# Optimization experiments

Measured on AMD Instinct MI355X. Metric: run time of the kernel, lower is better.

The kernel has to match this reference:

```python
import jax, jax.numpy as jnp
import numpy as np

N, E, IN_F, H, F = 4096, 131072, 512, 8, 32  # n_nodes, n_edges, in_features, n_heads, n_hidden
SLOPE = 0.2


def setup_inputs() -> dict:
    key = jax.random.key(0)
    k1, k2, k3, k4 = jax.random.split(key, 4)
    h = jax.random.normal(k1, (N, IN_F), dtype=jnp.float32)
    edge_index = jax.random.randint(k2, (2, E), 0, N)
    train_mask = jnp.ones((E + N,), dtype=jnp.float32)  # mask values written into adj (incl. self-loops appended in forward)
    W_fc = jax.random.normal(k3, (IN_F, H * F), dtype=jnp.float32) * (1.0 / np.sqrt(IN_F))
    W_attn = jax.random.normal(k4, (2 * F,), dtype=jnp.float32) * (1.0 / np.sqrt(2 * F))
    return {"h": h, "edge_index": edge_index, "train_mask": train_mask, "W_fc": W_fc, "W_attn": W_attn}


def reference(h, edge_index, train_mask, W_fc, W_attn):
    n = h.shape[0]
    g = (h @ W_fc).reshape(n, H, F)  # [n, H, F]
    # attn_fc(concat(g_i, g_j)) == g_i @ W_attn[:F] + g_j @ W_attn[F:]  (same math, no NxNx2F tensor)
    el = g @ W_attn[:F]  # [n, H], contribution of source row i
    er = g @ W_attn[F:]  # [n, H], contribution of column j
    e = jax.nn.leaky_relu(el[:, None, :] + er[None, :, :], SLOPE)  # [n, n, H]
    # adjacency: edges (+ self-loops appended in forward) get train_mask values, then diagonal forced to 1
    src = jnp.concatenate([edge_index[0], jnp.arange(n)])
    dst = jnp.concatenate([edge_index[1], jnp.arange(n)])
    adj = jnp.zeros((n, n), dtype=h.dtype).at[src, dst].set(train_mask)
    diag = jnp.arange(n)
    adj = adj.at[diag, diag].set(1.0)
    e = jnp.where(adj[:, :, None] == 0, -jnp.inf, e)
    a = jax.nn.softmax(e, axis=1)  # softmax over neighbors j (dropout p=0 -> identity)
    attn_res = jnp.einsum('ijh,jhf->ihf', a, g)  # [n, H, F]
    return attn_res.reshape(n, H * F)  # is_concat=True
```

## Files before the change

kernel.cpp:

```cpp
#include <hip/hip_runtime.h>
#include <stdint.h>

#define NN   4096
#define NE   131072
#define KIN  512
#define NH   8
#define HF   256
#define SLOPE 0.2f

typedef __attribute__((ext_vector_type(8))) short bf16x8;
typedef __attribute__((ext_vector_type(4))) float f32x4;


__device__ __forceinline__ unsigned short f2bf(float x) {
  unsigned u = __builtin_bit_cast(unsigned, x);
  u += 0x7FFFu + ((u >> 16) & 1u);
  return (unsigned short)(u >> 16);
}
__device__ __forceinline__ float bf2f(unsigned short x) {
  unsigned u = ((unsigned)x) << 16;
  return __builtin_bit_cast(float, u);
}

__global__ __launch_bounds__(256) void prep_k(const float* __restrict__ A,
                                              const float* __restrict__ B,
                                              unsigned* __restrict__ bitmap,
                                              unsigned short* __restrict__ Abf,
                                              unsigned short* __restrict__ Btbf) {
  __shared__ float tile[32][33];
  const int b = blockIdx.x, t = threadIdx.x;
  if (b < 512) {
    ((float4*)bitmap)[b * 256 + t] = make_float4(0.f, 0.f, 0.f, 0.f);
  } else if (b < 2560) {
    size_t idx = ((size_t)(b - 512) * 256 + t) * 4;
    float4 v = *(const float4*)&A[idx];
    ushort4 o;
    o.x = f2bf(v.x); o.y = f2bf(v.y); o.z = f2bf(v.z); o.w = f2bf(v.w);
    *(ushort4*)&Abf[idx] = o;
  } else {
    int bb = b - 2560;
    int k0 = (bb >> 3) * 32, n0 = (bb & 7) * 32;
    int lr = t >> 3, lc = (t & 7) * 4;
    float4 v = *(const float4*)&B[(size_t)(k0 + lr) * HF + n0 + lc];
    tile[lr][lc] = v.x; tile[lr][lc + 1] = v.y; tile[lr][lc + 2] = v.z; tile[lr][lc + 3] = v.w;
    __syncthreads();
    ushort4 o;
    o.x = f2bf(tile[lc + 0][lr]); o.y = f2bf(tile[lc + 1][lr]);
    o.z = f2bf(tile[lc + 2][lr]); o.w = f2bf(tile[lc + 3][lr]);
    *(ushort4*)&Btbf[(size_t)(n0 + lr) * KIN + k0 + lc] = o;
  }
}

__global__ __launch_bounds__(256) void gemm_adj_k(const unsigned short* __restrict__ A,
                                                  const unsigned short* __restrict__ Bt,
                                                  const float* __restrict__ Wa,
                                                  unsigned short* __restrict__ gbf,
                                                  float* __restrict__ el,
                                                  float* __restrict__ er,
                                                  const int* __restrict__ ei,
                                                  const float* __restrict__ mask,
                                                  unsigned* __restrict__ bitmap) {
  __shared__ unsigned short smem[2][4096];
  const int bx = blockIdx.x, t = threadIdx.x;
  if (bx >= 1024) {
    int k = (bx - 1024) * 256 + t;
    int s, d; float m;
    if (k < NE) { s = ei[k]; d = ei[NE + k]; m = mask[k]; }
    else        { s = k - NE; d = s; m = 1.0f; }
    if (m != 0.0f) atomicOr(&bitmap[s * 128 + (d >> 5)], 1u << (d & 31));
    return;
  }
  const int gx = bx & 127, gy = bx >> 7;
  const int row0 = gx * 32, col0 = gy * 32;
  const int w = t >> 6, l = t & 63;
  const int wr = w >> 1, wc = w & 1;

  const int srow = (w << 3) + (l >> 3);
  const int sch  = (l & 7) ^ (srow & 7);
  const unsigned short* gA = &A[(size_t)(row0 + srow) * KIN + sch * 8];
  const unsigned short* gB = &Bt[(size_t)(col0 + srow) * KIN + sch * 8];

#define STAGE(bf, ks)                                                                             \
  do {                                                                                            \
    __builtin_amdgcn_global_load_lds(                                                             \
        (const __attribute__((address_space(1))) unsigned int*)(gA + (size_t)(ks) * 64),          \
        (__attribute__((address_space(3))) unsigned int*)(&smem[bf][w * 512]), 16, 0, 0);         \
    __builtin_amdgcn_global_load_lds(                                                             \
        (const __attribute__((address_space(1))) unsigned int*)(gB + (size_t)(ks) * 64),          \
        (__attribute__((address_space(3))) unsigned int*)(&smem[bf][2048 + w * 512]), 16, 0, 0);  \
  } while (0)

  f32x4 acc = {};
  STAGE(0, 0);
  __syncthreads();
  const int lrow = l & 15, kg = l >> 4;
  const int ar = wr * 16 + lrow, br = wc * 16 + lrow;
  for (int ks = 0; ks < 8; ++ks) {
    const int bf = ks & 1;
    if (ks < 7) STAGE(bf ^ 1, ks + 1);
    bf16x8 a0 = *(const bf16x8*)&smem[bf][ar * 64 + ((kg ^ (ar & 7)) << 3)];
    bf16x8 a1 = *(const bf16x8*)&smem[bf][ar * 64 + (((4 + kg) ^ (ar & 7)) << 3)];
    bf16x8 b0 = *(const bf16x8*)&smem[bf][2048 + br * 64 + ((kg ^ (br & 7)) << 3)];
    bf16x8 b1 = *(const bf16x8*)&smem[bf][2048 + br * 64 + (((4 + kg) ^ (br & 7)) << 3)];
    acc = __builtin_amdgcn_mfma_f32_16x16x32_bf16(a0, b0, acc, 0, 0, 0);
    acc = __builtin_amdgcn_mfma_f32_16x16x32_bf16(a1, b1, acc, 0, 0, 0);
    __syncthreads();
  }
#undef STAGE

  const int crow = (l >> 4) * 4, ccol = l & 15;
  const int gr0 = row0 + wr * 16 + crow, gc = col0 + wc * 16 + ccol;
#pragma unroll
  for (int q = 0; q < 4; ++q) gbf[(size_t)(gr0 + q) * HF + gc] = f2bf(acc[q]);

  float* red = (float*)smem;
  const int f = wc * 16 + ccol;
  const float wal = Wa[f], war = Wa[32 + f];
#pragma unroll
  for (int q = 0; q < 4; ++q) {
    float pel = acc[q] * wal, per = acc[q] * war;
#pragma unroll
    for (int m = 8; m >= 1; m >>= 1) { pel += __shfl_xor(pel, m); per += __shfl_xor(per, m); }
    if (ccol == 0) {
      int rl = wr * 16 + crow + q;
      red[wc * 32 + rl] = pel;
      red[64 + wc * 32 + rl] = per;
    }
  }
  __syncthreads();
  if (t < 32) {
    el[(row0 + t) * NH + gy] = red[t] + red[32 + t];
    er[(row0 + t) * NH + gy] = red[64 + t] + red[96 + t];
  }
}

__global__ __launch_bounds__(256) void attn_k(const unsigned* __restrict__ bitmap,
                                              const unsigned short* __restrict__ gbf,
                                              const float* __restrict__ el_,
                                              const float* __restrict__ er_,
                                              float* __restrict__ out) {
  __shared__ unsigned short jl[NN];
  __shared__ float wlds[256 * NH];
  __shared__ int wtot[4];
  __shared__ int totalS;

  const int i = blockIdx.x;
  const int t = threadIdx.x;
  const int lane = t & 63;

  unsigned wbits = 0; int cnt = 0;
  if (t < 128) { wbits = bitmap[i * 128 + t]; cnt = __popc(wbits); }
  int incl = cnt;
#pragma unroll
  for (int d = 1; d < 64; d <<= 1) {
    int u = __shfl_up(incl, d);
    if (lane >= d) incl += u;
  }
  if (lane == 63) wtot[t >> 6] = incl;
  __syncthreads();
  int base = (t >= 64 && t < 128) ? wtot[0] : 0;
  if (t == 127) totalS = base + incl;
  if (t < 128) {
    int off = base + incl - cnt;
    unsigned ww = wbits;
    while (ww) {
      int b = __ffs(ww) - 1;
      jl[off++] = (unsigned short)(t * 32 + b);
      ww &= ww - 1;
    }
  }
  __syncthreads();
  const int total = totalS;

  const int hh = t >> 5;
  float acc = 0.f, den = 0.f;
  for (int c0 = 0; c0 < total; c0 += 256) {
    const int CL = min(256, total - c0);
    for (int p = t; p < CL * NH; p += 256) {
      int k = p >> 3, h2 = p & 7;
      int j = jl[c0 + k];
      float e  = el_[i * NH + h2] + er_[(size_t)j * NH + h2];
      float lr = e > 0.f ? e : SLOPE * e;
      wlds[p] = __expf(lr);
    }
    __syncthreads();
    int k = 0;
    for (; k + 4 <= CL; k += 4) {
      int j0 = jl[c0 + k], j1 = jl[c0 + k + 1], j2 = jl[c0 + k + 2], j3 = jl[c0 + k + 3];
      float g0 = bf2f(gbf[(size_t)j0 * HF + t]);
      float g1 = bf2f(gbf[(size_t)j1 * HF + t]);
      float g2 = bf2f(gbf[(size_t)j2 * HF + t]);
      float g3 = bf2f(gbf[(size_t)j3 * HF + t]);
      float w0 = wlds[(k + 0) * NH + hh], w1 = wlds[(k + 1) * NH + hh];
      float w2 = wlds[(k + 2) * NH + hh], w3 = wlds[(k + 3) * NH + hh];
      den += (w0 + w1) + (w2 + w3);
      acc += w0 * g0; acc += w1 * g1; acc += w2 * g2; acc += w3 * g3;
    }
    for (; k < CL; ++k) {
      int j0 = jl[c0 + k];
      float w0 = wlds[k * NH + hh];
      den += w0;
      acc += w0 * bf2f(gbf[(size_t)j0 * HF + t]);
    }
    __syncthreads();
  }
  out[(size_t)i * HF + t] = acc / den;
}

extern "C" void kernel_launch(void* const* d_in, const int* in_sizes, int n_in,
                              void* d_out, int out_size, void* d_ws, size_t ws_size,
                              hipStream_t stream) {
  const float* h      = (const float*)d_in[0];
  const int*   ei     = (const int*)d_in[1];
  const float* mask   = (const float*)d_in[2];
  const float* W_fc   = (const float*)d_in[3];
  const float* W_attn = (const float*)d_in[4];
  float* out = (float*)d_out;

  char* ws = (char*)d_ws;
  unsigned* bitmap      = (unsigned*)ws;
  unsigned short* gbf   = (unsigned short*)(ws + (size_t)2 * 1024 * 1024);
  float* el             = (float*)(ws + (size_t)4 * 1024 * 1024);
  float* er             = (float*)(ws + (size_t)4 * 1024 * 1024 + 128 * 1024);
  unsigned short* Abf   = (unsigned short*)(ws + (size_t)4 * 1024 * 1024 + 256 * 1024);
  unsigned short* Btbf  = (unsigned short*)(ws + (size_t)8 * 1024 * 1024 + 256 * 1024);

  prep_k<<<2688, 256, 0, stream>>>(h, W_fc, bitmap, Abf, Btbf);
  gemm_adj_k<<<1024 + 528, 256, 0, stream>>>(Abf, Btbf, W_attn, gbf, el, er, ei, mask, bitmap);
  attn_k<<<NN, 256, 0, stream>>>(bitmap, gbf, el, er, out);
}
```

Baseline: 37.03 us.

## Fuse fp32-to-bf16 conversion of h into GEMM and use one wave per node in attention

The GEMM now loads h as fp32 directly, converts it to bf16 in registers and writes it to LDS. This removes the separate prep pass over A, along with its 4 MB of writes and reads. The attention kernel now assigns one wavefront per node, with each lane covering 4 features. It computes the softmax weight inline per neighbour and drops the block-level LDS weight staging and its barriers. The trade-off is that every lane recomputes exp for its head, and the A loads move into the register-staged GEMM loop.

```diff
diff --git a/kernel.cpp b/kernel.cpp
--- a/kernel.cpp
+++ b/kernel.cpp
@@ -21,24 +21,19 @@
   unsigned u = ((unsigned)x) << 16;
   return __builtin_bit_cast(float, u);
 }
-
-__global__ __launch_bounds__(256) void prep_k(const float* __restrict__ A,
-                                              const float* __restrict__ B,
+__device__ __forceinline__ unsigned pack2(float lo, float hi) {
+  return (unsigned)f2bf(lo) | ((unsigned)f2bf(hi) << 16);
+}
+
+__global__ __launch_bounds__(256) void prep_k(const float* __restrict__ B,
                                               unsigned* __restrict__ bitmap,
-                                              unsigned short* __restrict__ Abf,
                                               unsigned short* __restrict__ Btbf) {
   __shared__ float tile[32][33];
   const int b = blockIdx.x, t = threadIdx.x;
   if (b < 512) {
     ((float4*)bitmap)[b * 256 + t] = make_float4(0.f, 0.f, 0.f, 0.f);
-  } else if (b < 2560) {
-    size_t idx = ((size_t)(b - 512) * 256 + t) * 4;
-    float4 v = *(const float4*)&A[idx];
-    ushort4 o;
-    o.x = f2bf(v.x); o.y = f2bf(v.y); o.z = f2bf(v.z); o.w = f2bf(v.w);
-    *(ushort4*)&Abf[idx] = o;
   } else {
-    int bb = b - 2560;
+    int bb = b - 512;
     int k0 = (bb >> 3) * 32, n0 = (bb & 7) * 32;
     int lr = t >> 3, lc = (t & 7) * 4;
     float4 v = *(const float4*)&B[(size_t)(k0 + lr) * HF + n0 + lc];
@@ -51,7 +46,7 @@
   }
 }
 
-__global__ __launch_bounds__(256) void gemm_adj_k(const unsigned short* __restrict__ A,
+__global__ __launch_bounds__(256) void gemm_adj_k(const float* __restrict__ h,
                                                   const unsigned short* __restrict__ Bt,
                                                   const float* __restrict__ Wa,
                                                   unsigned short* __restrict__ gbf,
@@ -76,37 +71,52 @@
   const int wr = w >> 1, wc = w & 1;
 
   const int srow = (w << 3) + (l >> 3);
-  const int sch  = (l & 7) ^ (srow & 7);
-  const unsigned short* gA = &A[(size_t)(row0 + srow) * KIN + sch * 8];
-  const unsigned short* gB = &Bt[(size_t)(col0 + srow) * KIN + sch * 8];
-
-#define STAGE(bf, ks)                                                                             \
-  do {                                                                                            \
-    __builtin_amdgcn_global_load_lds(                                                             \
-        (const __attribute__((address_space(1))) unsigned int*)(gA + (size_t)(ks) * 64),          \
-        (__attribute__((address_space(3))) unsigned int*)(&smem[bf][w * 512]), 16, 0, 0);         \
-    __builtin_amdgcn_global_load_lds(                                                             \
-        (const __attribute__((address_space(1))) unsigned int*)(gB + (size_t)(ks) * 64),          \
-        (__attribute__((address_space(3))) unsigned int*)(&smem[bf][2048 + w * 512]), 16, 0, 0);  \
-  } while (0)
+  const int sc   = l & 7;
+  const int aoff = srow * 64 + ((sc ^ (srow & 7)) << 3);
+  const float* gA = &h[(size_t)(row0 + srow) * KIN + sc * 8];
+  const int schB = sc ^ (srow & 7);
+  const unsigned short* gB = &Bt[(size_t)(col0 + srow) * KIN + schB * 8];
+
+#define BSTAGE(bf, ks)                                                                            \
+  __builtin_amdgcn_global_load_lds(                                                               \
+      (const __attribute__((address_space(1))) unsigned int*)(gB + (size_t)(ks) * 64),            \
+      (__attribute__((address_space(3))) unsigned int*)(&smem[bf][2048 + w * 512]), 16, 0, 0)
 
   f32x4 acc = {};
-  STAGE(0, 0);
+  {
+    float4 va0 = *(const float4*)(gA);
+    float4 va1 = *(const float4*)(gA + 4);
+    BSTAGE(0, 0);
+    uint4 w4 = {pack2(va0.x, va0.y), pack2(va0.z, va0.w),
+                pack2(va1.x, va1.y), pack2(va1.z, va1.w)};
+    *(uint4*)&smem[0][aoff] = w4;
+  }
   __syncthreads();
+
   const int lrow = l & 15, kg = l >> 4;
   const int ar = wr * 16 + lrow, br = wc * 16 + lrow;
   for (int ks = 0; ks < 8; ++ks) {
     const int bf = ks & 1;
-    if (ks < 7) STAGE(bf ^ 1, ks + 1);
+    float4 na0, na1;
+    if (ks < 7) {
+      na0 = *(const float4*)(gA + (ks + 1) * 64);
+      na1 = *(const float4*)(gA + (ks + 1) * 64 + 4);
+      BSTAGE(bf ^ 1, ks + 1);
+    }
     bf16x8 a0 = *(const bf16x8*)&smem[bf][ar * 64 + ((kg ^ (ar & 7)) << 3)];
     bf16x8 a1 = *(const bf16x8*)&smem[bf][ar * 64 + (((4 + kg) ^ (ar & 7)) << 3)];
     bf16x8 b0 = *(const bf16x8*)&smem[bf][2048 + br * 64 + ((kg ^ (br & 7)) << 3)];
     bf16x8 b1 = *(const bf16x8*)&smem[bf][2048 + br * 64 + (((4 + kg) ^ (br & 7)) << 3)];
     acc = __builtin_amdgcn_mfma_f32_16x16x32_bf16(a0, b0, acc, 0, 0, 0);
     acc = __builtin_amdgcn_mfma_f32_16x16x32_bf16(a1, b1, acc, 0, 0, 0);
+    if (ks < 7) {
+      uint4 w4 = {pack2(na0.x, na0.y), pack2(na0.z, na0.w),
+                  pack2(na1.x, na1.y), pack2(na1.z, na1.w)};
+      *(uint4*)&smem[bf ^ 1][aoff] = w4;
+    }
     __syncthreads();
   }
-#undef STAGE
+#undef BSTAGE
 
   const int crow = (l >> 4) * 4, ccol = l & 15;
   const int gr0 = row0 + wr * 16 + crow, gc = col0 + wc * 16 + ccol;
@@ -139,72 +149,47 @@
                                               const float* __restrict__ el_,
                                               const float* __restrict__ er_,
                                               float* __restrict__ out) {
-  __shared__ unsigned short jl[NN];
-  __shared__ float wlds[256 * NH];
-  __shared__ int wtot[4];
-  __shared__ int totalS;
-
-  const int i = blockIdx.x;
-  const int t = threadIdx.x;
-  const int lane = t & 63;
-
-  unsigned wbits = 0; int cnt = 0;
-  if (t < 128) { wbits = bitmap[i * 128 + t]; cnt = __popc(wbits); }
+  __shared__ unsigned short jl[4][NN];
+  const int t = threadIdx.x, wv = t >> 6, l = t & 63;
+  const int i = blockIdx.x * 4 + wv;
+
+  unsigned w0 = bitmap[i * 128 + l];
+  unsigned w1 = bitmap[i * 128 + 64 + l];
+  int cnt = __popc(w0) + __popc(w1);
   int incl = cnt;
 #pragma unroll
   for (int d = 1; d < 64; d <<= 1) {
     int u = __shfl_up(incl, d);
-    if (lane >= d) incl += u;
-  }
-  if (lane == 63) wtot[t >> 6] = incl;
+    if (l >= d) incl += u;
+  }
+  const int total = __shfl(incl, 63);
+  int off = incl - cnt;
+  unsigned short* J = jl[wv];
+  while (w0) { int b = __ffs(w0) - 1; J[off++] = (unsigned short)(l * 32 + b); w0 &= w0 - 1; }
+  while (w1) { int b = __ffs(w1) - 1; J[off++] = (unsigned short)((64 + l) * 32 + b); w1 &= w1 - 1; }
   __syncthreads();
-  int base = (t >= 64 && t < 128) ? wtot[0] : 0;
-  if (t == 127) totalS = base + incl;
-  if (t < 128) {
-    int off = base + incl - cnt;
-    unsigned ww = wbits;
-    while (ww) {
-      int b = __ffs(ww) - 1;
-      jl[off++] = (unsigned short)(t * 32 + b);
-      ww &= ww - 1;
-    }
-  }
-  __syncthreads();
-  const int total = totalS;
-
-  const int hh = t >> 5;
-  float acc = 0.f, den = 0.f;
-  for (int c0 = 0; c0 < total; c0 += 256) {
-    const int CL = min(256, total - c0);
-    for (int p = t; p < CL * NH; p += 256) {
-      int k = p >> 3, h2 = p & 7;
-      int j = jl[c0 + k];
-      float e  = el_[i * NH + h2] + er_[(size_t)j * NH + h2];
-      float lr = e > 0.f ? e : SLOPE * e;
-      wlds[p] = __expf(lr);
-    }
-    __syncthreads();
-    int k = 0;
-    for (; k + 4 <= CL; k += 4) {
-      int j0 = jl[c0 + k], j1 = jl[c0 + k + 1], j2 = jl[c0 + k + 2], j3 = jl[c0 + k + 3];
-      float g0 = bf2f(gbf[(size_t)j0 * HF + t]);
-      float g1 = bf2f(gbf[(size_t)j1 * HF + t]);
-      float g2 = bf2f(gbf[(size_t)j2 * HF + t]);
-      float g3 = bf2f(gbf[(size_t)j3 * HF + t]);
-      float w0 = wlds[(k + 0) * NH + hh], w1 = wlds[(k + 1) * NH + hh];
-      float w2 = wlds[(k + 2) * NH + hh], w3 = wlds[(k + 3) * NH + hh];
-      den += (w0 + w1) + (w2 + w3);
-      acc += w0 * g0; acc += w1 * g1; acc += w2 * g2; acc += w3 * g3;
-    }
-    for (; k < CL; ++k) {
-      int j0 = jl[c0 + k];
-      float w0 = wlds[k * NH + hh];
-      den += w0;
-      acc += w0 * bf2f(gbf[(size_t)j0 * HF + t]);
-    }
-    __syncthreads();
-  }
-  out[(size_t)i * HF + t] = acc / den;
+
+  const int hh = l >> 3;
+  const float elh = el_[i * NH + hh];
+  const unsigned short* gp = gbf + (size_t)l * 4;
+  f32x4 acc = {};
+  float den = 0.f;
+#pragma unroll 2
+  for (int k = 0; k < total; ++k) {
+    int j = J[k];
+    float e  = elh + er_[j * NH + hh];
+    float lr = e > 0.f ? e : SLOPE * e;
+    float wg = __expf(lr);
+    ushort4 gv = *(const ushort4*)(gp + (size_t)j * HF);
+    den += wg;
+    acc[0] += wg * bf2f(gv.x);
+    acc[1] += wg * bf2f(gv.y);
+    acc[2] += wg * bf2f(gv.z);
+    acc[3] += wg * bf2f(gv.w);
+  }
+  float inv = 1.f / den;
+  float4 o = make_float4(acc[0] * inv, acc[1] * inv, acc[2] * inv, acc[3] * inv);
+  *(float4*)&out[(size_t)i * HF + l * 4] = o;
 }
 
 extern "C" void kernel_launch(void* const* d_in, const int* in_sizes, int n_in,
@@ -222,10 +207,9 @@
   unsigned short* gbf   = (unsigned short*)(ws + (size_t)2 * 1024 * 1024);
   float* el             = (float*)(ws + (size_t)4 * 1024 * 1024);
   float* er             = (float*)(ws + (size_t)4 * 1024 * 1024 + 128 * 1024);
-  unsigned short* Abf   = (unsigned short*)(ws + (size_t)4 * 1024 * 1024 + 256 * 1024);
-  unsigned short* Btbf  = (unsigned short*)(ws + (size_t)8 * 1024 * 1024 + 256 * 1024);
-
-  prep_k<<<2688, 256, 0, stream>>>(h, W_fc, bitmap, Abf, Btbf);
-  gemm_adj_k<<<1024 + 528, 256, 0, stream>>>(Abf, Btbf, W_attn, gbf, el, er, ei, mask, bitmap);
-  attn_k<<<NN, 256, 0, stream>>>(bitmap, gbf, el, er, out);
-}
+  unsigned short* Btbf  = (unsigned short*)(ws + (size_t)4 * 1024 * 1024 + 256 * 1024);
+
+  prep_k<<<640, 256, 0, stream>>>(W_fc, bitmap, Btbf);
+  gemm_adj_k<<<1024 + 528, 256, 0, stream>>>(h, Btbf, W_attn, gbf, el, er, ei, mask, bitmap);
+  attn_k<<<NN / 4, 256, 0, stream>>>(bitmap, gbf, el, er, out);
+}
```

New measurement: 34.96 us. 5.6% less time.
